# Kernel tuning notes

Measured on AMD Instinct MI355X. Metric: run time of the kernel, lower is better.

The kernel has to match this reference:

```python
import jax, jax.numpy as jnp
import numpy as np

B, N, DIN, D, HID, C, K = 16, 1024, 768, 512, 128, 20, 64
H = W = 32
EPS = 1e-5  # BatchNorm eps (inference mode with running stats)


def _conv(x, w, pad=0, dil=1):
    return jax.lax.conv_general_dilated(
        x, w, (1, 1), [(pad, pad), (pad, pad)],
        rhs_dilation=(dil, dil),
        dimension_numbers=('NCHW', 'OIHW', 'NCHW'))


def _bn(x, g, b, m, v):
    inv = jax.lax.rsqrt(v + EPS)
    return (x - m[None, :, None, None]) * (g * inv)[None, :, None, None] + b[None, :, None, None]


def _l2norm(x):
    n = jnp.sqrt(jnp.sum(x * x, axis=-1, keepdims=True))
    return x / jnp.maximum(n, 1e-12)  # matches F.normalize(eps=1e-12)


def setup_inputs():
    key = jax.random.key(0)
    ks = jax.random.split(key, 12)

    def conv_w(k, o, i, kh, kw):
        return jax.random.normal(k, (o, i, kh, kw), jnp.float32) / np.sqrt(i * kh * kw)

    def bn_p(k, c):
        k1, k2 = jax.random.split(k)
        return (jnp.ones(c, jnp.float32), jnp.zeros(c, jnp.float32),
                0.1 * jax.random.normal(k1, (c,), jnp.float32),
                jax.random.uniform(k2, (c,), jnp.float32, 0.5, 1.5))

    g0, b0, m0, v0 = bn_p(ks[3], D)
    gr, br, mr, vr = bn_p(ks[4], HID)
    gl, bl, ml, vl = bn_p(ks[5], HID)
    gg, bg, mg, vg = bn_p(ks[6], HID)
    gp, bp, mp, vp = bn_p(ks[7], D)
    return {
        'patch_feats': jax.random.normal(ks[0], (B, N, DIN), jnp.float32),
        'protos': _l2norm(jax.random.normal(ks[1], (C, K, D), jnp.float32)),  # hybrid protos, L2-normed as in __init__
        'w0': conv_w(ks[2], D, DIN, 1, 1), 'g0': g0, 'b0': b0, 'm0': m0, 'v0': v0,
        'wr': conv_w(ks[8], HID, D, 1, 1), 'gr': gr, 'br': br, 'mr': mr, 'vr': vr,
        'wl': conv_w(ks[9], HID, HID, 3, 3), 'gl': gl, 'bl': bl, 'ml': ml, 'vl': vl,
        'wg': conv_w(ks[10], HID, HID, 3, 3), 'gg': gg, 'bg': bg, 'mg': mg, 'vg': vg,
        'wp': conv_w(ks[11], D, 2 * HID, 1, 1), 'gp': gp, 'bp': bp, 'mp': mp, 'vp': vp,
        'wf': conv_w(jax.random.fold_in(key, 99), D, D, 1, 1),
        'bf': jnp.zeros(D, jnp.float32),
        'logit_scale': jnp.float32(10.0),
    }


def reference(patch_feats, protos, w0, g0, b0, m0, v0, wr, gr, br, mr, vr,
              wl, gl, bl, ml, vl, wg, gg, bg, mg, vg, wp, gp, bp, mp, vp,
              wf, bf, logit_scale):
    Bq, Nq, Din = patch_feats.shape
    x = patch_feats.transpose(0, 2, 1).reshape(Bq, Din, H, W)
    # adapter: 1x1 conv -> BN -> ReLU
    x = jax.nn.relu(_bn(_conv(x, w0), g0, b0, m0, v0))
    # ResidualContextBlock
    res = x
    o = jax.nn.relu(_bn(_conv(x, wr), gr, br, mr, vr))
    l = jax.nn.relu(_bn(_conv(o, wl, pad=1), gl, bl, ml, vl))
    g = jax.nn.relu(_bn(_conv(o, wg, pad=2, dil=2), gg, bg, mg, vg))
    o = _bn(_conv(jnp.concatenate([l, g], axis=1), wp), gp, bp, mp, vp)
    x = jax.nn.relu(o + res)
    # final 1x1 conv (with bias)
    x = _conv(x, wf) + bf[None, :, None, None]
    # back to [B, N, D], L2 normalize
    x = x.reshape(Bq, D, Nq).transpose(0, 2, 1)
    x = _l2norm(x)
    # per-class cosine sims + double max reduction (vectorized over classes)
    sims = jnp.einsum('bnd,ckd->bcnk', x, protos)  # [B,C,N,K]
    A = sims.max(axis=-1)                          # [B,C,N] patch->proto max
    act_maps = A.reshape(Bq, C, H, W)
    logits = A.max(axis=-1) * logit_scale          # [B,C]
    return logits, act_maps, x
```

## Files before the change

### kernel.cpp

```cpp
#include <hip/hip_runtime.h>
#include <math.h>

#define BN_EPS 1e-5f

typedef __attribute__((ext_vector_type(8))) short short8v;
typedef __attribute__((ext_vector_type(8))) unsigned short ushort8v;
typedef __attribute__((ext_vector_type(4))) float f32x4;

__device__ __forceinline__ unsigned short f2b(float f) {
    unsigned int u = __float_as_uint(f);
    return (unsigned short)((u + 0x7FFFu + ((u >> 16) & 1u)) >> 16);
}
__device__ __forceinline__ float b2f(unsigned short h) {
    return __uint_as_float(((unsigned int)h) << 16);
}

typedef __attribute__((address_space(1))) const unsigned int gas_uint;
typedef __attribute__((address_space(3))) unsigned int las_uint;
__device__ __forceinline__ void gload16(const void* g, void* l) {
    __builtin_amdgcn_global_load_lds((gas_uint*)g, (las_uint*)l, 16, 0, 0);
}

#define VMCNT12() asm volatile("s_waitcnt vmcnt(12)" ::: "memory")
#define VMCNT8()  asm volatile("s_waitcnt vmcnt(8)"  ::: "memory")
#define VMCNT6()  asm volatile("s_waitcnt vmcnt(6)"  ::: "memory")
#define VMCNT4()  asm volatile("s_waitcnt vmcnt(4)"  ::: "memory")
#define VMCNT0()  asm volatile("s_waitcnt vmcnt(0)"  ::: "memory")
#define LGKM0()   asm volatile("s_waitcnt lgkmcnt(0)" ::: "memory")
#define SBAR()    __builtin_amdgcn_s_barrier()
#define SCHED0()  __builtin_amdgcn_sched_barrier(0)

__global__ __launch_bounds__(256) void f2b_kernel(
    const float* __restrict__ in, unsigned short* __restrict__ out, int n8)
{
    int i = blockIdx.x * 256 + threadIdx.x;
    if (i >= n8) return;
    const float4* p = (const float4*)(in + (size_t)i * 8);
    float4 a = p[0], b = p[1];
    ushort8v r;
    r[0] = f2b(a.x); r[1] = f2b(a.y); r[2] = f2b(a.z); r[3] = f2b(a.w);
    r[4] = f2b(b.x); r[5] = f2b(b.y); r[6] = f2b(b.z); r[7] = f2b(b.w);
    *(ushort8v*)(out + (size_t)i * 8) = r;
}

__global__ __launch_bounds__(256) void f2b_multi(
    const float* __restrict__ w0, const float* __restrict__ wr,
    const float* __restrict__ wp, const float* __restrict__ wf,
    const float* __restrict__ prot,
    unsigned short* __restrict__ w0o, unsigned short* __restrict__ wro,
    unsigned short* __restrict__ wpo, unsigned short* __restrict__ wfo,
    unsigned short* __restrict__ proto)
{
    int i = blockIdx.x * 256 + threadIdx.x;
    const float* src; unsigned short* dst; int off;
    if      (i <  49152) { src = w0;   dst = w0o;   off = i; }
    else if (i <  57344) { src = wr;   dst = wro;   off = i - 49152; }
    else if (i <  73728) { src = wp;   dst = wpo;   off = i - 57344; }
    else if (i < 106496) { src = wf;   dst = wfo;   off = i - 73728; }
    else if (i < 188416) { src = prot; dst = proto; off = i - 106496; }
    else return;
    const float4* p = (const float4*)(src + (size_t)off * 8);
    float4 a = p[0], b = p[1];
    ushort8v r;
    r[0] = f2b(a.x); r[1] = f2b(a.y); r[2] = f2b(a.z); r[3] = f2b(a.w);
    r[4] = f2b(b.x); r[5] = f2b(b.y); r[6] = f2b(b.z); r[7] = f2b(b.w);
    *(ushort8v*)(dst + (size_t)off * 8) = r;
}

__global__ __launch_bounds__(256) void convw_kernel(
    const float* __restrict__ wl, const float* __restrict__ wg,
    unsigned short* __restrict__ out)
{
    int i = blockIdx.x * 256 + threadIdx.x;
    if (i >= 294912) return;
    int br = i >= 147456;
    int j  = i - br * 147456;
    int tap = j >> 14, oc = (j >> 7) & 127, ic = j & 127;
    const float* src = br ? wg : wl;
    out[i] = f2b(src[((oc << 7) + ic) * 9 + tap]);
}

__global__ __launch_bounds__(256) void zero_kernel(unsigned short* __restrict__ p, int n8)
{
    int i = blockIdx.x * 256 + threadIdx.x;
    if (i >= n8) return;
    ushort8v z;
#pragma unroll
    for (int k = 0; k < 8; ++k) z[k] = 0;
    *(ushort8v*)(p + (size_t)i * 8) = z;
}

template <int EPI>
__global__ __launch_bounds__(256, 2) void mfma_gemm(
    const unsigned short* __restrict__ A, int lda,
    const unsigned short* __restrict__ Wt, int ldw,
    void* __restrict__ outp, int ldc, int Kdim,
    const float* __restrict__ bng, const float* __restrict__ bnb,
    const float* __restrict__ bnm, const float* __restrict__ bnv,
    const unsigned short* __restrict__ res, int ldres,
    const float* __restrict__ bias)
{
    __shared__ short8v Asta[4][512];
    __shared__ short8v Bsta[4][512];
    const int t  = threadIdx.x;
    const int l  = t & 63, wv = t >> 6;
    const int wm = wv >> 1, wn = wv & 1;
    const int m0 = blockIdx.x << 7, n0 = blockIdx.y << 7;

    const int r0  = t & 127;
    const int kb0 = t >> 7;

    const unsigned short* Ap = A  + (size_t)(m0 + r0) * lda + kb0 * 8;
    const unsigned short* Bp = Wt + (size_t)(n0 + r0) * ldw + kb0 * 8;

    f32x4 acc[4][4];
#pragma unroll
    for (int mf = 0; mf < 4; ++mf)
#pragma unroll
        for (int nf = 0; nf < 4; ++nf)
#pragma unroll
            for (int j = 0; j < 4; ++j) acc[mf][nf][j] = 0.f;

    const int arow = wm * 64 + (l & 15);
    const int brow = wn * 64 + (l & 15);
    const int kq   = l >> 4;

    const int nK = Kdim >> 5;

#define STAGE_G(buf, k0)                                     \
    do {                                                     \
        gload16(Ap + (k0),      &Asta[buf][wv * 64]);        \
        gload16(Ap + (k0) + 16, &Asta[buf][wv * 64 + 256]);  \
        gload16(Bp + (k0),      &Bsta[buf][wv * 64]);        \
        gload16(Bp + (k0) + 16, &Bsta[buf][wv * 64 + 256]);  \
    } while (0)

    STAGE_G(0, 0);
    STAGE_G(1, 32);
    STAGE_G(2, 64);
    for (int ks = 0; ks < nK; ++ks) {
        const int cb = ks & 3;
        if (ks + 3 < nK)       { STAGE_G((ks + 3) & 3, (ks + 3) << 5); VMCNT12(); }
        else if (ks + 3 == nK) { VMCNT8(); }
        else if (ks + 2 == nK) { VMCNT4(); }
        else                   { VMCNT0(); }
        SBAR();
        short8v af[4], bfv[4];
#pragma unroll
        for (int mf = 0; mf < 4; ++mf) af[mf]  = Asta[cb][kq * 128 + arow + mf * 16];
#pragma unroll
        for (int nf = 0; nf < 4; ++nf) bfv[nf] = Bsta[cb][kq * 128 + brow + nf * 16];
#pragma unroll
        for (int mf = 0; mf < 4; ++mf)
#pragma unroll
            for (int nf = 0; nf < 4; ++nf)
                acc[mf][nf] = __builtin_amdgcn_mfma_f32_16x16x32_bf16(
                    af[mf], bfv[nf], acc[mf][nf], 0, 0, 0);
        LGKM0(); SCHED0();
        SBAR();
    }
#undef STAGE_G

    float s[4], sh[4];
    int cols[4];
#pragma unroll
    for (int nf = 0; nf < 4; ++nf) {
        int col = n0 + wn * 64 + nf * 16 + (l & 15);
        cols[nf] = col;
        if (EPI == 2) { s[nf] = 1.f; sh[nf] = bias[col]; }
        else {
            float sc = bng[col] * rsqrtf(bnv[col] + BN_EPS);
            s[nf]  = sc;
            sh[nf] = bnb[col] - bnm[col] * sc;
        }
    }
#pragma unroll
    for (int mf = 0; mf < 4; ++mf) {
#pragma unroll
        for (int j = 0; j < 4; ++j) {
            int row = m0 + wm * 64 + mf * 16 + kq * 4 + j;
#pragma unroll
            for (int nf = 0; nf < 4; ++nf) {
                float v = acc[mf][nf][j] * s[nf] + sh[nf];
                if (EPI == 1) v += b2f(res[(size_t)row * ldres + cols[nf]]);
                if (EPI != 2) v = fmaxf(v, 0.f);
                if (EPI == 2) {
                    ((float*)outp)[(size_t)row * ldc + cols[nf]] = v;
                } else if (EPI == 3) {
                    int b = row >> 10, h = (row >> 5) & 31, ww = row & 31;
                    size_t pidx = ((size_t)(b * 36 + h + 2) * 36 + (ww + 2)) * 128 + cols[nf];
                    ((unsigned short*)outp)[pidx] = f2b(v);
                } else {
                    ((unsigned short*)outp)[(size_t)row * ldc + cols[nf]] = f2b(v);
                }
            }
        }
    }
}

__global__ __launch_bounds__(256, 2) void conv_mfma(
    const unsigned short* __restrict__ opad,
    const unsigned short* __restrict__ wt_all,
    const float* __restrict__ g1, const float* __restrict__ b1,
    const float* __restrict__ m1, const float* __restrict__ v1,
    const float* __restrict__ g2, const float* __restrict__ b2,
    const float* __restrict__ m2, const float* __restrict__ v2,
    unsigned short* __restrict__ lg)
{
    __shared__ short8v Asta[3][512];
    __shared__ short8v Bsta[3][1024];
    const int t = threadIdx.x;
    const int l = t & 63, wv = t >> 6;
    const int wm = wv >> 1, wn = wv & 1;
    const int m0 = blockIdx.x << 6;
    const int br = blockIdx.y;
    const int dil = 1 + br;
    const unsigned short* wtb = wt_all + (size_t)br * 147456;

    const int r0 = t & 63;
    const int m  = m0 + r0;
    const int bb = m >> 10, h = (m >> 5) & 31, wc = m & 31;
    const ptrdiff_t pbase = ((ptrdiff_t)(bb * 36 + h + 2) * 36 + (wc + 2)) * 128;
    const unsigned short* ApT = opad + pbase + (t >> 6) * 8;
    const unsigned short* BpT = wtb + (size_t)(t & 127) * 128 + (t >> 7) * 8;

    f32x4 acc[2][4];
#pragma unroll
    for (int mf = 0; mf < 2; ++mf)
#pragma unroll
        for (int nf = 0; nf < 4; ++nf)
#pragma unroll
            for (int j = 0; j < 4; ++j) acc[mf][nf][j] = 0.f;

    const int arow = wm * 32 + (l & 15);
    const int bcol = wn * 64 + (l & 15);
    const int kq   = l >> 4;

#define STAGE_C(buf, s)                                                        \
    do {                                                                       \
        int tap_ = (s) >> 1, hh_ = ((s) & 1) * 64;                             \
        int dh_ = tap_ / 3 - 1, dw_ = tap_ % 3 - 1;                            \
        const unsigned short* Ap_ = ApT + (ptrdiff_t)((dh_ * 36 + dw_) * dil) * 128 + hh_; \
        const unsigned short* Bp_ = BpT + (size_t)tap_ * 16384 + hh_;          \
        gload16(Ap_,      &Asta[buf][wv * 64]);                                \
        gload16(Ap_ + 32, &Asta[buf][wv * 64 + 256]);                          \
        gload16(Bp_,      &Bsta[buf][wv * 64]);                                \
        gload16(Bp_ + 16, &Bsta[buf][wv * 64 + 256]);                          \
        gload16(Bp_ + 32, &Bsta[buf][wv * 64 + 512]);                          \
        gload16(Bp_ + 48, &Bsta[buf][wv * 64 + 768]);                          \
    } while (0)

    STAGE_C(0, 0);
    STAGE_C(1, 1);
    int cb = 0;
    for (int s = 0; s < 18; ++s) {
        int sb = cb + 2; if (sb >= 3) sb -= 3;
        if (s + 2 < 18)       { STAGE_C(sb, s + 2); VMCNT12(); }
        else if (s + 2 == 18) { VMCNT6(); }
        else                  { VMCNT0(); }
        SBAR();
        short8v af[2][2], bfv[2][4];
#pragma unroll
        for (int kk = 0; kk < 2; ++kk) {
            int kb = kk * 4 + kq;
            af[kk][0] = Asta[cb][kb * 64 + arow];
            af[kk][1] = Asta[cb][kb * 64 + arow + 16];
#pragma unroll
            for (int nf = 0; nf < 4; ++nf)
                bfv[kk][nf] = Bsta[cb][kb * 128 + bcol + nf * 16];
        }
#pragma unroll
        for (int kk = 0; kk < 2; ++kk)
#pragma unroll
            for (int mf = 0; mf < 2; ++mf)
#pragma unroll
                for (int nf = 0; nf < 4; ++nf)
                    acc[mf][nf] = __builtin_amdgcn_mfma_f32_16x16x32_bf16(
                        af[kk][mf], bfv[kk][nf], acc[mf][nf], 0, 0, 0);
        LGKM0(); SCHED0();
        SBAR();
        cb += 1; if (cb >= 3) cb -= 3;
    }
#undef STAGE_C

    const float* gg = br ? g2 : g1;
    const float* gb = br ? b2 : b1;
    const float* gm = br ? m2 : m1;
    const float* gv = br ? v2 : v1;
    float s4[4], sh[4];
    int cols[4];
#pragma unroll
    for (int nf = 0; nf < 4; ++nf) {
        int col = bcol + nf * 16;
        cols[nf] = col;
        float sc = gg[col] * rsqrtf(gv[col] + BN_EPS);
        s4[nf] = sc;
        sh[nf] = gb[col] - gm[col] * sc;
    }
#pragma unroll
    for (int mf = 0; mf < 2; ++mf) {
#pragma unroll
        for (int j = 0; j < 4; ++j) {
            int row = m0 + wm * 32 + mf * 16 + kq * 4 + j;
#pragma unroll
            for (int nf = 0; nf < 4; ++nf) {
                float v = fmaxf(acc[mf][nf][j] * s4[nf] + sh[nf], 0.f);
                lg[(size_t)row * 256 + br * 128 + cols[nf]] = f2b(v);
            }
        }
    }
}

__global__ __launch_bounds__(256) void l2norm_rows(
    float* __restrict__ x, unsigned short* __restrict__ xn)
{
    const int t    = threadIdx.x;
    const int wv   = t >> 6, lane = t & 63;
    const int row  = (blockIdx.x << 2) + wv;
    float* p = x + (size_t)row * 512 + (lane << 3);
    float4 a = *(float4*)p;
    float4 b = *(float4*)(p + 4);
    float ss = a.x * a.x + a.y * a.y + a.z * a.z + a.w * a.w +
               b.x * b.x + b.y * b.y + b.z * b.z + b.w * b.w;
#pragma unroll
    for (int off = 32; off >= 1; off >>= 1) ss += __shfl_xor(ss, off);
    float sc = 1.f / fmaxf(sqrtf(ss), 1e-12f);
    a.x *= sc; a.y *= sc; a.z *= sc; a.w *= sc;
    b.x *= sc; b.y *= sc; b.z *= sc; b.w *= sc;
    *(float4*)p       = a;
    *(float4*)(p + 4) = b;
    ushort8v r;
    r[0] = f2b(a.x); r[1] = f2b(a.y); r[2] = f2b(a.z); r[3] = f2b(a.w);
    r[4] = f2b(b.x); r[5] = f2b(b.y); r[6] = f2b(b.z); r[7] = f2b(b.w);
    *(ushort8v*)(xn + (size_t)row * 512 + (lane << 3)) = r;
}

__global__ __launch_bounds__(256, 2) void sims_mfma(
    const unsigned short* __restrict__ xn,
    const unsigned short* __restrict__ protos,
    float* __restrict__ act)
{
    __shared__ short8v Asta[4][512];
    __shared__ short8v Bsta[4][512];
    const int t = threadIdx.x;
    const int l = t & 63, wv = t >> 6;
    const int wm = wv >> 1, wn = wv & 1;
    const int m0 = blockIdx.x << 7;

    const int r0  = t & 127, kb0 = t >> 7;
    const unsigned short* Ap = xn + (size_t)(m0 + r0) * 512 + kb0 * 8;
    const unsigned short* Bp = protos + ((size_t)blockIdx.y * 128 + r0) * 512 + kb0 * 8;

    f32x4 acc[4][4];
#pragma unroll
    for (int mf = 0; mf < 4; ++mf)
#pragma unroll
        for (int nf = 0; nf < 4; ++nf)
#pragma unroll
            for (int j = 0; j < 4; ++j) acc[mf][nf][j] = 0.f;

    const int arow = wm * 64 + (l & 15);
    const int brow = wn * 64 + (l & 15);
    const int kq   = l >> 4;

#define STAGE_S(buf, k0)                                     \
    do {                                                     \
        gload16(Ap + (k0),      &Asta[buf][wv * 64]);        \
        gload16(Ap + (k0) + 16, &Asta[buf][wv * 64 + 256]);  \
        gload16(Bp + (k0),      &Bsta[buf][wv * 64]);        \
        gload16(Bp + (k0) + 16, &Bsta[buf][wv * 64 + 256]);  \
    } while (0)

    STAGE_S(0, 0);
    STAGE_S(1, 32);
    STAGE_S(2, 64);
    for (int ks = 0; ks < 16; ++ks) {
        const int cb = ks & 3;
        if (ks + 3 < 16)       { STAGE_S((ks + 3) & 3, (ks + 3) << 5); VMCNT12(); }
        else if (ks + 3 == 16) { VMCNT8(); }
        else if (ks + 2 == 16) { VMCNT4(); }
        else                   { VMCNT0(); }
        SBAR();
        short8v af[4], bfv[4];
#pragma unroll
        for (int mf = 0; mf < 4; ++mf) af[mf]  = Asta[cb][kq * 128 + arow + mf * 16];
#pragma unroll
        for (int nf = 0; nf < 4; ++nf) bfv[nf] = Bsta[cb][kq * 128 + brow + nf * 16];
#pragma unroll
        for (int mf = 0; mf < 4; ++mf)
#pragma unroll
            for (int nf = 0; nf < 4; ++nf)
                acc[mf][nf] = __builtin_amdgcn_mfma_f32_16x16x32_bf16(
                    af[mf], bfv[nf], acc[mf][nf], 0, 0, 0);
        LGKM0(); SCHED0();
        SBAR();
    }
#undef STAGE_S

    const int c = (blockIdx.y << 1) + wn;
#pragma unroll
    for (int mf = 0; mf < 4; ++mf) {
        float vj[4];
#pragma unroll
        for (int j = 0; j < 4; ++j) {
            float v = fmaxf(fmaxf(acc[mf][0][j], acc[mf][1][j]),
                            fmaxf(acc[mf][2][j], acc[mf][3][j]));
            v = fmaxf(v, __shfl_xor(v, 1));
            v = fmaxf(v, __shfl_xor(v, 2));
            v = fmaxf(v, __shfl_xor(v, 4));
            v = fmaxf(v, __shfl_xor(v, 8));
            vj[j] = v;
        }
        if ((l & 15) == 0) {
            int rowb = m0 + wm * 64 + mf * 16 + kq * 4;
#pragma unroll
            for (int j = 0; j < 4; ++j) {
                int row = rowb + j;
                int bb = row >> 10, n = row & 1023;
                act[(((size_t)(bb * 20 + c)) << 10) + n] = vj[j];
            }
        }
    }
}

__global__ __launch_bounds__(256) void logits_max(
    const float* __restrict__ act, const float* __restrict__ lsc,
    float* __restrict__ logits)
{
    const int bc = blockIdx.x;
    const int t  = threadIdx.x;
    float4 v = *(const float4*)(act + ((size_t)bc << 10) + (t << 2));
    float mx = fmaxf(fmaxf(v.x, v.y), fmaxf(v.z, v.w));
#pragma unroll
    for (int off = 32; off >= 1; off >>= 1) mx = fmaxf(mx, __shfl_xor(mx, off));
    __shared__ float wmred[4];
    if ((t & 63) == 0) wmred[t >> 6] = mx;
    __syncthreads();
    if (t == 0) {
        float m2 = fmaxf(fmaxf(wmred[0], wmred[1]), fmaxf(wmred[2], wmred[3]));
        logits[bc] = m2 * lsc[0];
    }
}

extern "C" void kernel_launch(void* const* d_in, const int* in_sizes, int n_in,
                              void* d_out, int out_size, void* d_ws, size_t ws_size,
                              hipStream_t stream)
{
    const float* pf   = (const float*)d_in[0];
    const float* prot = (const float*)d_in[1];
    const float* w0   = (const float*)d_in[2];
    const float* g0   = (const float*)d_in[3];
    const float* b0   = (const float*)d_in[4];
    const float* m0v  = (const float*)d_in[5];
    const float* v0   = (const float*)d_in[6];
    const float* wr   = (const float*)d_in[7];
    const float* gr   = (const float*)d_in[8];
    const float* br   = (const float*)d_in[9];
    const float* mr   = (const float*)d_in[10];
    const float* vr   = (const float*)d_in[11];
    const float* wl   = (const float*)d_in[12];
    const float* gl   = (const float*)d_in[13];
    const float* bl   = (const float*)d_in[14];
    const float* ml   = (const float*)d_in[15];
    const float* vl   = (const float*)d_in[16];
    const float* wg   = (const float*)d_in[17];
    const float* gG   = (const float*)d_in[18];
    const float* bG   = (const float*)d_in[19];
    const float* mG   = (const float*)d_in[20];
    const float* vG   = (const float*)d_in[21];
    const float* wp   = (const float*)d_in[22];
    const float* gp   = (const float*)d_in[23];
    const float* bp   = (const float*)d_in[24];
    const float* mp   = (const float*)d_in[25];
    const float* vp   = (const float*)d_in[26];
    const float* wf   = (const float*)d_in[27];
    const float* bf_  = (const float*)d_in[28];
    const float* lsc  = (const float*)d_in[29];

    char* ws = (char*)d_ws;
    unsigned short* pf_bf    = (unsigned short*)(ws);
    unsigned short* w0_bf    = (unsigned short*)(ws + 25165824);
    unsigned short* wr_bf    = (unsigned short*)(ws + 25952256);
    unsigned short* wt_bf    = (unsigned short*)(ws + 26083328);
    unsigned short* wp_bf    = (unsigned short*)(ws + 26673152);
    unsigned short* wf_bf    = (unsigned short*)(ws + 26935296);
    unsigned short* prot_bf  = (unsigned short*)(ws + 27459584);
    unsigned short* x1_bf    = (unsigned short*)(ws + 28770304);
    unsigned short* opad     = (unsigned short*)(ws + 45547520);
    unsigned short* lg_bf    = (unsigned short*)(ws + 50855936);
    unsigned short* x2_bf    = (unsigned short*)(ws + 59244544);
    unsigned short* xn_bf    = (unsigned short*)(ws + 76021760);

    float* out    = (float*)d_out;
    float* logits = out;
    float* act    = out + 320;
    float* xo     = out + 328000;

    f2b_kernel<<<6144, 256, 0, stream>>>(pf, pf_bf, 1572864);
    f2b_multi<<<736, 256, 0, stream>>>(w0, wr, wp, wf, prot,
                                       w0_bf, wr_bf, wp_bf, wf_bf, prot_bf);
    convw_kernel<<<1152, 256, 0, stream>>>(wl, wg, wt_bf);
    zero_kernel<<<1296, 256, 0, stream>>>(opad, 331776);

    mfma_gemm<0><<<dim3(128, 4), 256, 0, stream>>>(
        pf_bf, 768, w0_bf, 768, x1_bf, 512, 768,
        g0, b0, m0v, v0, nullptr, 0, nullptr);

    mfma_gemm<3><<<dim3(128, 1), 256, 0, stream>>>(
        x1_bf, 512, wr_bf, 512, opad, 0, 512,
        gr, br, mr, vr, nullptr, 0, nullptr);

    conv_mfma<<<dim3(256, 2), 256, 0, stream>>>(
        opad, wt_bf, gl, bl, ml, vl, gG, bG, mG, vG, lg_bf);

    mfma_gemm<1><<<dim3(128, 4), 256, 0, stream>>>(
        lg_bf, 256, wp_bf, 256, x2_bf, 512, 256,
        gp, bp, mp, vp, x1_bf, 512, nullptr);

    mfma_gemm<2><<<dim3(128, 4), 256, 0, stream>>>(
        x2_bf, 512, wf_bf, 512, xo, 512, 512,
        nullptr, nullptr, nullptr, nullptr, nullptr, 0, bf_);

    l2norm_rows<<<4096, 256, 0, stream>>>(xo, xn_bf);

    sims_mfma<<<dim3(128, 10), 256, 0, stream>>>(xn_bf, prot_bf, act);

    logits_max<<<320, 256, 0, stream>>>(act, lsc, logits);
}
```

Before: 202.0 us.

## Use 512-thread blocks with double buffering in GEMM and sims kernels

```diff
diff --git a/kernel.cpp b/kernel.cpp
--- a/kernel.cpp
+++ b/kernel.cpp
@@ -21,10 +21,9 @@
     __builtin_amdgcn_global_load_lds((gas_uint*)g, (las_uint*)l, 16, 0, 0);
 }
 
-#define VMCNT12() asm volatile("s_waitcnt vmcnt(12)" ::: "memory")
-#define VMCNT8()  asm volatile("s_waitcnt vmcnt(8)"  ::: "memory")
+#define VMCNT2()  asm volatile("s_waitcnt vmcnt(2)"  ::: "memory")
+#define VMCNT3()  asm volatile("s_waitcnt vmcnt(3)"  ::: "memory")
 #define VMCNT6()  asm volatile("s_waitcnt vmcnt(6)"  ::: "memory")
-#define VMCNT4()  asm volatile("s_waitcnt vmcnt(4)"  ::: "memory")
 #define VMCNT0()  asm volatile("s_waitcnt vmcnt(0)"  ::: "memory")
 #define LGKM0()   asm volatile("s_waitcnt lgkmcnt(0)" ::: "memory")
 #define SBAR()    __builtin_amdgcn_s_barrier()
@@ -91,7 +90,7 @@
 }
 
 template <int EPI>
-__global__ __launch_bounds__(256, 2) void mfma_gemm(
+__global__ __launch_bounds__(512, 8) void mfma_gemm(
     const unsigned short* __restrict__ A, int lda,
     const unsigned short* __restrict__ Wt, int ldw,
     void* __restrict__ outp, int ldc, int Kdim,
@@ -100,8 +99,8 @@
     const unsigned short* __restrict__ res, int ldres,
     const float* __restrict__ bias)
 {
-    __shared__ short8v Asta[4][512];
-    __shared__ short8v Bsta[4][512];
+    __shared__ short8v Asta[2][512];
+    __shared__ short8v Bsta[2][512];
     const int t  = threadIdx.x;
     const int l  = t & 63, wv = t >> 6;
     const int wm = wv >> 1, wn = wv & 1;
@@ -109,49 +108,42 @@
 
     const int r0  = t & 127;
     const int kb0 = t >> 7;
-
     const unsigned short* Ap = A  + (size_t)(m0 + r0) * lda + kb0 * 8;
     const unsigned short* Bp = Wt + (size_t)(n0 + r0) * ldw + kb0 * 8;
 
-    f32x4 acc[4][4];
-#pragma unroll
-    for (int mf = 0; mf < 4; ++mf)
+    f32x4 acc[2][4];
+#pragma unroll
+    for (int mf = 0; mf < 2; ++mf)
 #pragma unroll
         for (int nf = 0; nf < 4; ++nf)
 #pragma unroll
             for (int j = 0; j < 4; ++j) acc[mf][nf][j] = 0.f;
 
-    const int arow = wm * 64 + (l & 15);
+    const int arow = wm * 32 + (l & 15);
     const int brow = wn * 64 + (l & 15);
     const int kq   = l >> 4;
 
     const int nK = Kdim >> 5;
 
-#define STAGE_G(buf, k0)                                     \
-    do {                                                     \
-        gload16(Ap + (k0),      &Asta[buf][wv * 64]);        \
-        gload16(Ap + (k0) + 16, &Asta[buf][wv * 64 + 256]);  \
-        gload16(Bp + (k0),      &Bsta[buf][wv * 64]);        \
-        gload16(Bp + (k0) + 16, &Bsta[buf][wv * 64 + 256]);  \
+#define STAGE_G(buf, k0)                          \
+    do {                                          \
+        gload16(Ap + (k0), &Asta[buf][wv * 64]);  \
+        gload16(Bp + (k0), &Bsta[buf][wv * 64]);  \
     } while (0)
 
     STAGE_G(0, 0);
-    STAGE_G(1, 32);
-    STAGE_G(2, 64);
     for (int ks = 0; ks < nK; ++ks) {
-        const int cb = ks & 3;
-        if (ks + 3 < nK)       { STAGE_G((ks + 3) & 3, (ks + 3) << 5); VMCNT12(); }
-        else if (ks + 3 == nK) { VMCNT8(); }
-        else if (ks + 2 == nK) { VMCNT4(); }
-        else                   { VMCNT0(); }
+        const int cb = ks & 1;
+        if (ks + 1 < nK) { STAGE_G(cb ^ 1, (ks + 1) << 5); VMCNT2(); }
+        else             { VMCNT0(); }
         SBAR();
-        short8v af[4], bfv[4];
-#pragma unroll
-        for (int mf = 0; mf < 4; ++mf) af[mf]  = Asta[cb][kq * 128 + arow + mf * 16];
+        short8v af[2], bfv[4];
+#pragma unroll
+        for (int mf = 0; mf < 2; ++mf) af[mf]  = Asta[cb][kq * 128 + arow + mf * 16];
 #pragma unroll
         for (int nf = 0; nf < 4; ++nf) bfv[nf] = Bsta[cb][kq * 128 + brow + nf * 16];
 #pragma unroll
-        for (int mf = 0; mf < 4; ++mf)
+        for (int mf = 0; mf < 2; ++mf)
 #pragma unroll
             for (int nf = 0; nf < 4; ++nf)
                 acc[mf][nf] = __builtin_amdgcn_mfma_f32_16x16x32_bf16(
@@ -175,10 +167,10 @@
         }
     }
 #pragma unroll
-    for (int mf = 0; mf < 4; ++mf) {
+    for (int mf = 0; mf < 2; ++mf) {
 #pragma unroll
         for (int j = 0; j < 4; ++j) {
-            int row = m0 + wm * 64 + mf * 16 + kq * 4 + j;
+            int row = m0 + wm * 32 + mf * 16 + kq * 4 + j;
 #pragma unroll
             for (int nf = 0; nf < 4; ++nf) {
                 float v = acc[mf][nf][j] * s[nf] + sh[nf];
@@ -255,7 +247,8 @@
     int cb = 0;
     for (int s = 0; s < 18; ++s) {
         int sb = cb + 2; if (sb >= 3) sb -= 3;
-        if (s + 2 < 18)       { STAGE_C(sb, s + 2); VMCNT12(); }
+        if (s + 2 < 18)       { STAGE_C(sb, s + 2);
+                                asm volatile("s_waitcnt vmcnt(12)" ::: "memory"); }
         else if (s + 2 == 18) { VMCNT6(); }
         else                  { VMCNT0(); }
         SBAR();
@@ -335,21 +328,21 @@
     *(ushort8v*)(xn + (size_t)row * 512 + (lane << 3)) = r;
 }
 
-__global__ __launch_bounds__(256, 2) void sims_mfma(
+__global__ __launch_bounds__(512, 6) void sims_mfma(
     const unsigned short* __restrict__ xn,
     const unsigned short* __restrict__ protos,
     float* __restrict__ act)
 {
-    __shared__ short8v Asta[4][512];
-    __shared__ short8v Bsta[4][512];
+    __shared__ short8v Asta[2][512];
+    __shared__ short8v Bsta[2][1024];
     const int t = threadIdx.x;
     const int l = t & 63, wv = t >> 6;
-    const int wm = wv >> 1, wn = wv & 1;
+    const int wm = wv >> 2, wn = wv & 3;
     const int m0 = blockIdx.x << 7;
 
-    const int r0  = t & 127, kb0 = t >> 7;
-    const unsigned short* Ap = xn + (size_t)(m0 + r0) * 512 + kb0 * 8;
-    const unsigned short* Bp = protos + ((size_t)blockIdx.y * 128 + r0) * 512 + kb0 * 8;
+    const unsigned short* Ap = xn + (size_t)(m0 + (t & 127)) * 512 + (t >> 7) * 8;
+    const unsigned short* Bp = protos +
+        ((size_t)blockIdx.y * 256 + (t & 255)) * 512 + (t >> 8) * 8;
 
     f32x4 acc[4][4];
 #pragma unroll
@@ -366,26 +359,21 @@
 #define STAGE_S(buf, k0)                                     \
     do {                                                     \
         gload16(Ap + (k0),      &Asta[buf][wv * 64]);        \
-        gload16(Ap + (k0) + 16, &Asta[buf][wv * 64 + 256]);  \
         gload16(Bp + (k0),      &Bsta[buf][wv * 64]);        \
-        gload16(Bp + (k0) + 16, &Bsta[buf][wv * 64 + 256]);  \
+        gload16(Bp + (k0) + 16, &Bsta[buf][wv * 64 + 512]);  \
     } while (0)
 
     STAGE_S(0, 0);
-    STAGE_S(1, 32);
-    STAGE_S(2, 64);
     for (int ks = 0; ks < 16; ++ks) {
-        const int cb = ks & 3;
-        if (ks + 3 < 16)       { STAGE_S((ks + 3) & 3, (ks + 3) << 5); VMCNT12(); }
-        else if (ks + 3 == 16) { VMCNT8(); }
-        else if (ks + 2 == 16) { VMCNT4(); }
-        else                   { VMCNT0(); }
+        const int cb = ks & 1;
+        if (ks + 1 < 16) { STAGE_S(cb ^ 1, (ks + 1) << 5); VMCNT3(); }
+        else             { VMCNT0(); }
         SBAR();
         short8v af[4], bfv[4];
 #pragma unroll
         for (int mf = 0; mf < 4; ++mf) af[mf]  = Asta[cb][kq * 128 + arow + mf * 16];
 #pragma unroll
-        for (int nf = 0; nf < 4; ++nf) bfv[nf] = Bsta[cb][kq * 128 + brow + nf * 16];
+        for (int nf = 0; nf < 4; ++nf) bfv[nf] = Bsta[cb][kq * 256 + brow + nf * 16];
 #pragma unroll
         for (int mf = 0; mf < 4; ++mf)
 #pragma unroll
@@ -397,7 +385,7 @@
     }
 #undef STAGE_S
 
-    const int c = (blockIdx.y << 1) + wn;
+    const int c = blockIdx.y * 4 + wn;
 #pragma unroll
     for (int mf = 0; mf < 4; ++mf) {
         float vj[4];
@@ -502,28 +490,28 @@
     convw_kernel<<<1152, 256, 0, stream>>>(wl, wg, wt_bf);
     zero_kernel<<<1296, 256, 0, stream>>>(opad, 331776);
 
-    mfma_gemm<0><<<dim3(128, 4), 256, 0, stream>>>(
+    mfma_gemm<0><<<dim3(128, 4), 512, 0, stream>>>(
         pf_bf, 768, w0_bf, 768, x1_bf, 512, 768,
         g0, b0, m0v, v0, nullptr, 0, nullptr);
 
-    mfma_gemm<3><<<dim3(128, 1), 256, 0, stream>>>(
+    mfma_gemm<3><<<dim3(128, 1), 512, 0, stream>>>(
         x1_bf, 512, wr_bf, 512, opad, 0, 512,
         gr, br, mr, vr, nullptr, 0, nullptr);
 
     conv_mfma<<<dim3(256, 2), 256, 0, stream>>>(
         opad, wt_bf, gl, bl, ml, vl, gG, bG, mG, vG, lg_bf);
 
-    mfma_gemm<1><<<dim3(128, 4), 256, 0, stream>>>(
+    mfma_gemm<1><<<dim3(128, 4), 512, 0, stream>>>(
         lg_bf, 256, wp_bf, 256, x2_bf, 512, 256,
         gp, bp, mp, vp, x1_bf, 512, nullptr);
 
-    mfma_gemm<2><<<dim3(128, 4), 256, 0, stream>>>(
+    mfma_gemm<2><<<dim3(128, 4), 512, 0, stream>>>(
         x2_bf, 512, wf_bf, 512, xo, 512, 512,
         nullptr, nullptr, nullptr, nullptr, nullptr, 0, bf_);
 
     l2norm_rows<<<4096, 256, 0, stream>>>(xo, xn_bf);
 
-    sims_mfma<<<dim3(128, 10), 256, 0, stream>>>(xn_bf, prot_bf, act);
+    sims_mfma<<<dim3(128, 5), 512, 0, stream>>>(xn_bf, prot_bf, act);
 
     logits_max<<<320, 256, 0, stream>>>(act, lsc, logits);
 }
```

Result: slower. 298.5 us (+47.8%).
